# Performance work log

Hardware: AMD Instinct MI355X
Metric: run time of the kernel (lower is better)

The kernel has to match this reference:

```python
import jax, jax.numpy as jnp
import numpy as np

N = 20000      # nodes
E = 320000     # edges (before self loops)
IN = 128       # in_channels
HID = 64       # hid_channels
H = 4          # in_head
OUT = 16       # out_channels (classes)
SLOPE = 0.2    # GATv2 leaky_relu negative_slope default


def setup_inputs() -> dict:
    key = jax.random.key(0)
    ks = jax.random.split(key, 40)
    d = {}
    d["x"] = jax.random.normal(ks[0], (N, IN), jnp.float32)
    src = jax.random.randint(ks[1], (E,), 0, N)
    dst = jax.random.randint(ks[2], (E,), 0, N)
    d["edge_index"] = jnp.stack([src, dst]).astype(jnp.int32)
    # (in_ch, out_ch_per_head, heads) for the 4 GATv2Conv layers
    dims = [(IN, HID, H), (H * HID, HID, H), (H * HID, HID, H), (H * HID, OUT, 1)]
    ki = 3
    for li, (ic, oc, h) in enumerate(dims, 1):
        sc = 1.0 / np.sqrt(ic)
        d[f"w{li}l"] = jax.random.normal(ks[ki], (h * oc, ic), jnp.float32) * sc; ki += 1
        d[f"b{li}l"] = jnp.zeros((h * oc,), jnp.float32)
        d[f"w{li}r"] = jax.random.normal(ks[ki], (h * oc, ic), jnp.float32) * sc; ki += 1
        d[f"b{li}r"] = jnp.zeros((h * oc,), jnp.float32)
        d[f"a{li}"] = jax.random.normal(ks[ki], (h, oc), jnp.float32) * (1.0 / np.sqrt(oc)); ki += 1
        # output bias: [h*oc] if concat else [oc]; layer 4 is concat=False
        d[f"bo{li}"] = jnp.zeros((h * oc if li < 4 else oc,), jnp.float32)
    return d


def gatv2_layer(x, src, dst, wl, bl, wr, br, att, bias, heads, oc, concat):
    n = x.shape[0]
    xl = (x @ wl.T + bl).reshape(n, heads, oc)   # source transform
    xr = (x @ wr.T + br).reshape(n, heads, oc)   # target transform
    # per-edge GATv2 attention logit: a^T LeakyReLU(x_l[src] + x_r[dst])
    e = jax.nn.leaky_relu(xl[src] + xr[dst], SLOPE)          # [E,H,C]
    logits = jnp.einsum('ehc,hc->eh', e, att)                # [E,H]
    # segment softmax over incoming edges of each dst node
    m = jax.ops.segment_max(logits, dst, num_segments=n)     # [N,H]
    ex = jnp.exp(logits - m[dst])
    den = jax.ops.segment_sum(ex, dst, num_segments=n)
    alpha = ex / den[dst]                                    # [E,H]
    out = jax.ops.segment_sum(alpha[..., None] * xl[src], dst, num_segments=n)  # [N,H,C]
    out = out.reshape(n, heads * oc) if concat else out.mean(axis=1)
    return out + bias


def reference(x, edge_index,
              w1l, b1l, w1r, b1r, a1, bo1,
              w2l, b2l, w2r, b2r, a2, bo2,
              w3l, b3l, w3r, b3r, a3, bo3,
              w4l, b4l, w4r, b4r, a4, bo4):
    n = x.shape[0]
    loop = jnp.arange(n, dtype=edge_index.dtype)
    src = jnp.concatenate([edge_index[0], loop])  # PyG GATv2Conv adds self loops
    dst = jnp.concatenate([edge_index[1], loop])
    h = gatv2_layer(x, src, dst, w1l, b1l, w1r, b1r, a1, bo1, H, HID, True)
    h = jax.nn.relu(h)
    h = gatv2_layer(h, src, dst, w2l, b2l, w2r, b2r, a2, bo2, H, HID, True)
    h = jax.nn.relu(h)
    h = gatv2_layer(h, src, dst, w3l, b3l, w3r, b3r, a3, bo3, H, HID, True)
    h = jax.nn.relu(h)
    h = gatv2_layer(h, src, dst, w4l, b4l, w4r, b4r, a4, bo4, 1, OUT, False)
    return h
```

## Files before the change

kernel.cpp:

```cpp
#include <hip/hip_runtime.h>
#include <hip/hip_bf16.h>
#include <math.h>

#define NNODES 20000
#define NEDGES 320000
#define ETOT   (NEDGES + NNODES)
#define SLOPE  0.2f
#define MAXDEG 96

typedef __attribute__((ext_vector_type(8))) short bf16x8;
typedef __attribute__((ext_vector_type(4))) float f32x4;

__device__ inline unsigned short bfbits(float f) {
    __hip_bfloat16 h = __float2bfloat16(f);
    unsigned short u;
    __builtin_memcpy(&u, &h, 2);
    return u;
}
__device__ inline float bf2f(unsigned short u) {
    __hip_bfloat16 h;
    __builtin_memcpy(&h, &u, 2);
    return __bfloat162float(h);
}

__global__ void slab_fill(const int* __restrict__ ei, int* __restrict__ fill,
                          int* __restrict__ slab) {
    int idx = blockIdx.x * blockDim.x + threadIdx.x;
    if (idx >= ETOT) return;
    int src, dst;
    if (idx < NEDGES) { src = ei[idx]; dst = ei[NEDGES + idx]; }
    else              { src = idx - NEDGES; dst = src; }
    int pos = atomicAdd(&fill[dst], 1);
    if (pos < MAXDEG) slab[dst * MAXDEG + pos] = src;
}

__global__ void bin_hist(const int* __restrict__ fill, int* __restrict__ bcnt) {
    __shared__ int h[32];
    const int t = threadIdx.x;
    if (t < 32) h[t] = 0;
    __syncthreads();
    int n = blockIdx.x * 256 + t;
    if (n < NNODES) atomicAdd(&h[min(fill[n], 31)], 1);
    __syncthreads();
    if (t < 32 && h[t] > 0) atomicAdd(&bcnt[t], h[t]);
}

__global__ void bin_scan(const int* __restrict__ bcnt, int* __restrict__ bfill) {
    if (threadIdx.x == 0) {
        int run = 0;
        for (int i = 0; i < 32; i++) { bfill[i] = run; run += bcnt[i]; }
    }
}

__global__ void bin_place(const int* __restrict__ fill, int* __restrict__ bfill,
                          int* __restrict__ order) {
    __shared__ int h[32];
    __shared__ int base[32];
    const int t = threadIdx.x;
    if (t < 32) h[t] = 0;
    __syncthreads();
    int n = blockIdx.x * 256 + t;
    int bin = 0, loc = 0;
    if (n < NNODES) {
        bin = min(fill[n], 31);
        loc = atomicAdd(&h[bin], 1);
    }
    __syncthreads();
    if (t < 32) base[t] = (h[t] > 0) ? atomicAdd(&bfill[t], h[t]) : 0;
    __syncthreads();
    if (n < NNODES) order[base[bin] + loc] = n;
}

__global__ void convert_x(const float* __restrict__ x, unsigned short* __restrict__ Ap) {
    int idx = blockIdx.x * 256 + threadIdx.x;
    if (idx >= NNODES * 128) return;
    int m = idx >> 7, k = idx & 127;
    float f = x[idx];
    unsigned short hi = bfbits(f);
    unsigned short lo = bfbits(f - bf2f(hi));
    unsigned short* row = Ap + (size_t)m * 256;
    row[k] = hi; row[128 + k] = lo;
}

__global__ void convert_w(const float* __restrict__ w0, const float* __restrict__ w1,
                          unsigned short* __restrict__ Wp, int K, int n0, int ntot) {
    int idx = blockIdx.x * 256 + threadIdx.x;
    if (idx >= ntot * K) return;
    int n = idx / K, k = idx - n * K;
    float f = (n < n0) ? w0[n * K + k] : w1[(n - n0) * K + k];
    unsigned short hi = bfbits(f);
    unsigned short lo = bfbits(f - bf2f(hi));
    unsigned short* row = Wp + (size_t)n * 2 * K;
    row[k] = hi; row[K + k] = lo;
}

template <int NOUT, int KK>
__global__ __launch_bounds__(64) void gemm_reg(
    const unsigned short* __restrict__ Ap,
    const unsigned short* __restrict__ Wp,
    const float* __restrict__ bias0, const float* __restrict__ bias1,
    float* __restrict__ O0, float* __restrict__ O1)
{
    constexpr int S  = KK / 32;
    constexpr int NF = (NOUT == 512) ? 4 : 2;

    int m0, n0;
    if constexpr (NOUT == 512) {
        const int xcd  = blockIdx.x & 7;
        const int idx  = blockIdx.x >> 3;
        const int nblk = idx & 7;
        const int mg   = idx >> 3;
        const int mp   = mg * 8 + xcd;
        if (mp >= (NNODES + 63) / 64) return;
        m0 = mp * 64;
        n0 = nblk * 64;
    } else {
        m0 = blockIdx.x * 64;
        n0 = 0;
    }

    const int l   = threadIdx.x;
    const int lr  = l & 15;
    const int lkb = (l >> 4) * 16;

    const char* ab = (const char*)Ap;
    const char* bb = (const char*)Wp;

    unsigned aoff[4], boff[NF];
    #pragma unroll
    for (int f = 0; f < 4; f++) {
        int row = min(m0 + f * 16 + lr, NNODES - 1);
        aoff[f] = (unsigned)row * (unsigned)(4 * KK) + (unsigned)lkb;
    }
    #pragma unroll
    for (int f = 0; f < NF; f++) {
        int row = n0 + f * 16 + lr;
        boff[f] = (unsigned)row * (unsigned)(4 * KK) + (unsigned)lkb;
    }

    f32x4 acc[4][NF];
    #pragma unroll
    for (int i = 0; i < 4; i++)
        #pragma unroll
        for (int j = 0; j < NF; j++)
            acc[i][j] = (f32x4){0.f, 0.f, 0.f, 0.f};

    bf16x8 fa[2][8];
    bf16x8 fb[2][2 * NF];

    auto LD = [&](int buf, int s) {
        const unsigned kb = (unsigned)s * 64;
        #pragma unroll
        for (int f = 0; f < 4; f++) {
            fa[buf][f]     = *(const bf16x8*)(ab + aoff[f] + kb);
            fa[buf][4 + f] = *(const bf16x8*)(ab + aoff[f] + (unsigned)(2 * KK) + kb);
        }
        #pragma unroll
        for (int f = 0; f < NF; f++) {
            fb[buf][f]      = *(const bf16x8*)(bb + boff[f] + kb);
            fb[buf][NF + f] = *(const bf16x8*)(bb + boff[f] + (unsigned)(2 * KK) + kb);
        }
    };

    auto COMP = [&](int buf) {
        #pragma unroll
        for (int mi = 0; mi < 4; mi++)
            #pragma unroll
            for (int ni = 0; ni < NF; ni++) {
                acc[mi][ni] = __builtin_amdgcn_mfma_f32_16x16x32_bf16(
                    fa[buf][mi], fb[buf][ni], acc[mi][ni], 0, 0, 0);
                acc[mi][ni] = __builtin_amdgcn_mfma_f32_16x16x32_bf16(
                    fa[buf][mi], fb[buf][NF + ni], acc[mi][ni], 0, 0, 0);
                acc[mi][ni] = __builtin_amdgcn_mfma_f32_16x16x32_bf16(
                    fa[buf][4 + mi], fb[buf][ni], acc[mi][ni], 0, 0, 0);
            }
    };

    LD(0, 0);
    #pragma unroll
    for (int s = 0; s < S; ++s) {
        if (s + 1 < S) LD((s + 1) & 1, s + 1);
        COMP(s & 1);
    }

    #pragma unroll
    for (int mi = 0; mi < 4; mi++) {
        int r0 = m0 + mi * 16 + (l >> 4) * 4;
        #pragma unroll
        for (int ni = 0; ni < NF; ni++) {
            int c = n0 + ni * 16 + (l & 15);
            if constexpr (NOUT == 512) {
                const bool left = (c < 256);
                float*       O  = left ? O0 : O1;
                const int    cc = left ? c : c - 256;
                const float  bv = left ? bias0[cc] : bias1[cc];
                const int head = cc >> 6, ch = cc & 63;
                #pragma unroll
                for (int r = 0; r < 4; r++) {
                    int m = r0 + r;
                    if (m < NNODES)
                        O[((size_t)head * NNODES + m) * 64 + ch] = acc[mi][ni][r] + bv;
                }
            } else {
                const float bv = (c < 16) ? bias0[c] : bias1[c - 16];
                #pragma unroll
                for (int r = 0; r < 4; r++) {
                    int m = r0 + r;
                    if (m < NNODES) O0[(size_t)m * 32 + c] = acc[mi][ni][r] + bv;
                }
            }
        }
    }
}

__device__ inline float edge_score(float4 v, float4 xrv, float4 attv) {
    float tx = v.x + xrv.x; tx = fmaxf(tx, SLOPE * tx);
    float ty = v.y + xrv.y; ty = fmaxf(ty, SLOPE * ty);
    float tz = v.z + xrv.z; tz = fmaxf(tz, SLOPE * tz);
    float tw = v.w + xrv.w; tw = fmaxf(tw, SLOPE * tw);
    float s = attv.x * tx + attv.y * ty + attv.z * tz + attv.w * tw;
    s += __shfl_xor(s, 1, 64);
    s += __shfl_xor(s, 2, 64);
    s += __shfl_xor(s, 4, 64);
    s += __shfl_xor(s, 8, 64);
    return s;
}

__device__ inline void sm_upd(float s, float4 v, bool act,
                              float& m, float& den, float4& acc) {
    float d = s - m;
    bool  r = act && (d > 8.f);
    float e = __expf(r ? -d : d);
    float sc = r ? e : 1.f;
    float pw = act ? (r ? 1.f : e) : 0.f;
    m = r ? s : m;
    den = den * sc + pw;
    acc.x = acc.x * sc + pw * v.x;
    acc.y = acc.y * sc + pw * v.y;
    acc.z = acc.z * sc + pw * v.z;
    acc.w = acc.w * sc + pw * v.w;
}

__device__ inline void sm_merge(float& m0, float& den0, float4& acc0,
                                float m1, float den1, float4 acc1) {
    float nm = fmaxf(m0, m1);
    float sa = __expf(m0 - nm);
    float sb = __expf(m1 - nm);
    den0 = den0 * sa + den1 * sb;
    acc0.x = acc0.x * sa + acc1.x * sb;
    acc0.y = acc0.y * sa + acc1.y * sb;
    acc0.z = acc0.z * sa + acc1.z * sb;
    acc0.w = acc0.w * sa + acc1.w * sb;
    m0 = nm;
}

__global__ __launch_bounds__(64) void gat_attn_head(
    const float* __restrict__ xl, const float* __restrict__ xr,
    const float* __restrict__ att, const float* __restrict__ bo,
    const int* __restrict__ fill, const int* __restrict__ slab,
    const int* __restrict__ order,
    unsigned short* __restrict__ outp)
{
    const int b    = blockIdx.x;
    const int xcd  = b & 7;
    const int head = xcd >> 1;
    const int grp  = (b >> 3) * 2 + (xcd & 1);
    const int lane = threadIdx.x;
    const int sub  = lane >> 4;
    const int c    = lane & 15;

    const int node = order[grp * 4 + sub];
    const unsigned coff = (unsigned)c << 4;

    const char* xlh = (const char*)xl + (size_t)head * (NNODES * 256);
    const char* xrh = (const char*)xr + (size_t)head * (NNODES * 256);

    const float4 attv = *(const float4*)&att[head * 64 + c * 4];
    const float4 xrv  = *(const float4*)(xrh + ((unsigned)node << 8) + coff);
    const float4 bov  = *(const float4*)&bo[head * 64 + c * 4];

    const int  deg = min(fill[node], MAXDEG);
    const int* sl  = slab + node * MAXDEG;

    int maxd = deg;
    maxd = max(maxd, __shfl_xor(maxd, 16, 64));
    maxd = max(maxd, __shfl_xor(maxd, 32, 64));

    float  m0 = -1e30f, m1 = -1e30f, m2 = -1e30f, m3 = -1e30f;
    float  d0 = 0.f, d1 = 0.f, d2 = 0.f, d3 = 0.f;
    float4 a0 = make_float4(0.f, 0.f, 0.f, 0.f);
    float4 a1 = a0, a2 = a0, a3 = a0;

    auto gather = [&](int src) -> float4 {
        return *(const float4*)(xlh + (((unsigned)src << 8) + coff));
    };

    auto batch = [&](float4 v0, float4 v1, float4 v2, float4 v3, int pb) {
        const bool A0 = pb + 0 < deg, A1 = pb + 1 < deg;
        const bool A2 = pb + 2 < deg, A3 = pb + 3 < deg;
        float s0 = edge_score(v0, xrv, attv);
        float s1 = edge_score(v1, xrv, attv);
        float s2 = edge_score(v2, xrv, attv);
        float s3 = edge_score(v3, xrv, attv);
        bool need = (A0 & (s0 - m0 > 8.f)) | (A1 & (s1 - m1 > 8.f)) |
                    (A2 & (s2 - m2 > 8.f)) | (A3 & (s3 - m3 > 8.f));
        if (!__any(need)) {
            float p0 = A0 ? __expf(s0 - m0) : 0.f;
            float p1 = A1 ? __expf(s1 - m1) : 0.f;
            float p2 = A2 ? __expf(s2 - m2) : 0.f;
            float p3 = A3 ? __expf(s3 - m3) : 0.f;
            d0 += p0; d1 += p1; d2 += p2; d3 += p3;
            a0.x += p0 * v0.x; a0.y += p0 * v0.y; a0.z += p0 * v0.z; a0.w += p0 * v0.w;
            a1.x += p1 * v1.x; a1.y += p1 * v1.y; a1.z += p1 * v1.z; a1.w += p1 * v1.w;
            a2.x += p2 * v2.x; a2.y += p2 * v2.y; a2.z += p2 * v2.z; a2.w += p2 * v2.w;
            a3.x += p3 * v3.x; a3.y += p3 * v3.y; a3.z += p3 * v3.z; a3.w += p3 * v3.w;
        } else {
            sm_upd(s0, v0, A0, m0, d0, a0);
            sm_upd(s1, v1, A1, m1, d1, a1);
            sm_upd(s2, v2, A2, m2, d2, a2);
            sm_upd(s3, v3, A3, m3, d3, a3);
        }
    };

    int4 s4 = *(const int4*)sl;
    float4 v0 = gather((0 < deg) ? s4.x : node);
    float4 v1 = gather((1 < deg) ? s4.y : node);
    float4 v2 = gather((2 < deg) ? s4.z : node);
    float4 v3 = gather((3 < deg) ? s4.w : node);
    int pc = 0;
    for (int p = 4; p < maxd; p += 4) {
        int4 t4 = *(const int4*)&sl[p];
        float4 w0 = gather((p + 0 < deg) ? t4.x : node);
        float4 w1 = gather((p + 1 < deg) ? t4.y : node);
        float4 w2 = gather((p + 2 < deg) ? t4.z : node);
        float4 w3 = gather((p + 3 < deg) ? t4.w : node);
        batch(v0, v1, v2, v3, pc);
        v0 = w0; v1 = w1; v2 = w2; v3 = w3;
        pc = p;
    }
    batch(v0, v1, v2, v3, pc);

    sm_merge(m0, d0, a0, m1, d1, a1);
    sm_merge(m2, d2, a2, m3, d3, a3);
    sm_merge(m0, d0, a0, m2, d2, a2);

    float4 o;
    o.x = fmaxf(a0.x / d0 + bov.x, 0.f);
    o.y = fmaxf(a0.y / d0 + bov.y, 0.f);
    o.z = fmaxf(a0.z / d0 + bov.z, 0.f);
    o.w = fmaxf(a0.w / d0 + bov.w, 0.f);

    unsigned short* row = outp + (size_t)node * 512 + head * 64 + c * 4;
    ushort4 hv, lv;
    hv.x = bfbits(o.x); hv.y = bfbits(o.y); hv.z = bfbits(o.z); hv.w = bfbits(o.w);
    lv.x = bfbits(o.x - bf2f(hv.x));
    lv.y = bfbits(o.y - bf2f(hv.y));
    lv.z = bfbits(o.z - bf2f(hv.z));
    lv.w = bfbits(o.w - bf2f(hv.w));
    *(ushort4*)(row)       = hv;
    *(ushort4*)(row + 256) = lv;
}

__global__ __launch_bounds__(128) void gat_attn_final(
    const float* __restrict__ O32,
    const float* __restrict__ att, const float* __restrict__ bo,
    const int* __restrict__ fill, const int* __restrict__ slab,
    float* __restrict__ out)
{
    const int lane = threadIdx.x & 63;
    const int sub  = lane >> 4;
    const int c    = lane & 15;

    const int node = (blockIdx.x * 2 + (threadIdx.x >> 6)) * 4 + sub;
    if (node >= NNODES) return;

    const unsigned coff = (unsigned)c << 2;
    const char*    ob   = (const char*)O32;

    const float attc = att[c];
    const float xrc  = *(const float*)(ob + (((unsigned)node << 7) + 64 + coff));

    const int  deg = min(fill[node], MAXDEG);
    const int* sl  = slab + node * MAXDEG;

    float m0 = -1e30f, m1 = -1e30f, d0 = 0.f, d1 = 0.f, a0 = 0.f, a1 = 0.f;

    int p = 0;
    for (; p + 2 <= deg; p += 2) {
        int srcA = sl[p];
        int srcB = sl[p + 1];
        float vA = *(const float*)(ob + (((unsigned)srcA << 7) + coff));
        float vB = *(const float*)(ob + (((unsigned)srcB << 7) + coff));
        float tA = vA + xrc; tA = fmaxf(tA, SLOPE * tA);
        float tB = vB + xrc; tB = fmaxf(tB, SLOPE * tB);
        float sA = attc * tA;
        float sB = attc * tB;
        sA += __shfl_xor(sA, 1, 64);  sB += __shfl_xor(sB, 1, 64);
        sA += __shfl_xor(sA, 2, 64);  sB += __shfl_xor(sB, 2, 64);
        sA += __shfl_xor(sA, 4, 64);  sB += __shfl_xor(sB, 4, 64);
        sA += __shfl_xor(sA, 8, 64);  sB += __shfl_xor(sB, 8, 64);
        {
            float dd = sA - m0; bool r = dd > 8.f;
            float e = __expf(r ? -dd : dd);
            float sc = r ? e : 1.f, pw = r ? 1.f : e;
            m0 = r ? sA : m0;
            d0 = d0 * sc + pw;
            a0 = a0 * sc + pw * vA;
        }
        {
            float dd = sB - m1; bool r = dd > 8.f;
            float e = __expf(r ? -dd : dd);
            float sc = r ? e : 1.f, pw = r ? 1.f : e;
            m1 = r ? sB : m1;
            d1 = d1 * sc + pw;
            a1 = a1 * sc + pw * vB;
        }
    }
    if (p < deg) {
        int src = sl[p];
        float v = *(const float*)(ob + (((unsigned)src << 7) + coff));
        float t = v + xrc; t = fmaxf(t, SLOPE * t);
        float s = attc * t;
        s += __shfl_xor(s, 1, 64);
        s += __shfl_xor(s, 2, 64);
        s += __shfl_xor(s, 4, 64);
        s += __shfl_xor(s, 8, 64);
        float dd = s - m0; bool r = dd > 8.f;
        float e = __expf(r ? -dd : dd);
        float sc = r ? e : 1.f, pw = r ? 1.f : e;
        m0 = r ? s : m0;
        d0 = d0 * sc + pw;
        a0 = a0 * sc + pw * v;
    }

    float nm = fmaxf(m0, m1);
    float sa = __expf(m0 - nm);
    float sb = __expf(m1 - nm);
    float den = d0 * sa + d1 * sb;
    out[(size_t)node * 16 + c] = (a0 * sa + a1 * sb) / den + bo[c];
}

extern "C" void kernel_launch(void* const* d_in, const int* in_sizes, int n_in,
                              void* d_out, int out_size, void* d_ws, size_t ws_size,
                              hipStream_t stream)
{
    const float* x   = (const float*)d_in[0];
    const int*   ei  = (const int*)d_in[1];
    const float* w1l = (const float*)d_in[2];  const float* b1l = (const float*)d_in[3];
    const float* w1r = (const float*)d_in[4];  const float* b1r = (const float*)d_in[5];
    const float* a1  = (const float*)d_in[6];  const float* bo1 = (const float*)d_in[7];
    const float* w2l = (const float*)d_in[8];  const float* b2l = (const float*)d_in[9];
    const float* w2r = (const float*)d_in[10]; const float* b2r = (const float*)d_in[11];
    const float* a2  = (const float*)d_in[12]; const float* bo2 = (const float*)d_in[13];
    const float* w3l = (const float*)d_in[14]; const float* b3l = (const float*)d_in[15];
    const float* w3r = (const float*)d_in[16]; const float* b3r = (const float*)d_in[17];
    const float* a3  = (const float*)d_in[18]; const float* bo3 = (const float*)d_in[19];
    const float* w4l = (const float*)d_in[20]; const float* b4l = (const float*)d_in[21];
    const float* w4r = (const float*)d_in[22]; const float* b4r = (const float*)d_in[23];
    const float* a4  = (const float*)d_in[24]; const float* bo4 = (const float*)d_in[25];

    char* ws = (char*)d_ws;
    auto carve = [&](size_t bytes) {
        void* p = ws;
        ws += (bytes + 255) & ~(size_t)255;
        return p;
    };
    unsigned short* Ap = (unsigned short*)carve((size_t)NNODES * 512 * sizeof(unsigned short));
    float* xl = (float*)carve((size_t)NNODES * 256 * sizeof(float));
    float* xr = (float*)carve((size_t)NNODES * 256 * sizeof(float));
    float* O32 = xl;
    unsigned short* Wp1 = (unsigned short*)carve((size_t)512 * 256 * sizeof(unsigned short));
    unsigned short* Wp2 = (unsigned short*)carve((size_t)512 * 512 * sizeof(unsigned short));
    unsigned short* Wp3 = (unsigned short*)carve((size_t)512 * 512 * sizeof(unsigned short));
    unsigned short* Wp4 = (unsigned short*)carve((size_t)32 * 512 * sizeof(unsigned short));
    int* fill  = (int*)carve((size_t)NNODES * sizeof(int));
    int* slab  = (int*)carve((size_t)NNODES * MAXDEG * sizeof(int));
    int* bcnt  = (int*)carve(32 * sizeof(int));
    int* bfill = (int*)carve(32 * sizeof(int));
    int* order = (int*)carve((size_t)NNODES * sizeof(int));

    const int eblocks = (ETOT + 255) / 256;
    const int nblocks = (NNODES + 255) / 256;

    convert_x<<<(NNODES * 128 + 255) / 256, 256, 0, stream>>>(x, Ap);
    convert_w<<<(512 * 128 + 255) / 256, 256, 0, stream>>>(w1l, w1r, Wp1, 128, 256, 512);
    convert_w<<<(512 * 256 + 255) / 256, 256, 0, stream>>>(w2l, w2r, Wp2, 256, 256, 512);
    convert_w<<<(512 * 256 + 255) / 256, 256, 0, stream>>>(w3l, w3r, Wp3, 256, 256, 512);
    convert_w<<<(32 * 256 + 255) / 256, 256, 0, stream>>>(w4l, w4r, Wp4, 256, 16, 32);

    hipMemsetAsync(fill, 0, (size_t)NNODES * sizeof(int), stream);
    hipMemsetAsync(bcnt, 0, 32 * sizeof(int), stream);
    slab_fill<<<eblocks, 256, 0, stream>>>(ei, fill, slab);
    bin_hist<<<nblocks, 256, 0, stream>>>(fill, bcnt);
    bin_scan<<<1, 64, 0, stream>>>(bcnt, bfill);
    bin_place<<<nblocks, 256, 0, stream>>>(fill, bfill, order);

    const int g512 = 2560;
    const int g32  = (NNODES + 63) / 64;
    const int ah   = 20000;

    gemm_reg<512, 128><<<g512, 64, 0, stream>>>(Ap, Wp1, b1l, b1r, xl, xr);
    gat_attn_head<<<ah, 64, 0, stream>>>(xl, xr, a1, bo1, fill, slab, order, Ap);

    gemm_reg<512, 256><<<g512, 64, 0, stream>>>(Ap, Wp2, b2l, b2r, xl, xr);
    gat_attn_head<<<ah, 64, 0, stream>>>(xl, xr, a2, bo2, fill, slab, order, Ap);

    gemm_reg<512, 256><<<g512, 64, 0, stream>>>(Ap, Wp3, b3l, b3r, xl, xr);
    gat_attn_head<<<ah, 64, 0, stream>>>(xl, xr, a3, bo3, fill, slab, order, Ap);

    gemm_reg<32, 256><<<g32, 64, 0, stream>>>(Ap, Wp4, b4l, b4r, O32, O32);
    gat_attn_final<<<(NNODES + 7) / 8, 128, 0, stream>>>(O32, a4, bo4, fill, slab, (float*)d_out);
}
```

Baseline: 307.6 us.

## Stage GEMM tiles through LDS with direct global-to-LDS loads across four waves

Replaces the single-wave register-blocked GEMM with a 256-thread block. Its four waves cooperatively stage 64x32 A and B tiles (hi and lo bf16 parts) into double-buffered shared memory using global_load_lds. Each wave then computes a 32x32 sub-tile from LDS. This is meant to cut redundant global loads and raise per-block parallelism, at the cost of a block barrier every k-step. For the 32-wide final layer, half of the waves compute columns that are then discarded.

```diff
diff --git a/kernel.cpp b/kernel.cpp
--- a/kernel.cpp
+++ b/kernel.cpp
@@ -21,6 +21,12 @@
     __hip_bfloat16 h;
     __builtin_memcpy(&h, &u, 2);
     return __bfloat162float(h);
+}
+
+__device__ inline void gload_lds16(const unsigned short* g, unsigned short* s) {
+    __builtin_amdgcn_global_load_lds(
+        (const __attribute__((address_space(1))) unsigned int*)g,
+        (__attribute__((address_space(3))) unsigned int*)s, 16, 0, 0);
 }
 
 __global__ void slab_fill(const int* __restrict__ ei, int* __restrict__ fill,
@@ -95,14 +101,19 @@
 }
 
 template <int NOUT, int KK>
-__global__ __launch_bounds__(64) void gemm_reg(
+__global__ __launch_bounds__(256) void gemm_lds(
     const unsigned short* __restrict__ Ap,
     const unsigned short* __restrict__ Wp,
     const float* __restrict__ bias0, const float* __restrict__ bias1,
     float* __restrict__ O0, float* __restrict__ O1)
 {
-    constexpr int S  = KK / 32;
-    constexpr int NF = (NOUT == 512) ? 4 : 2;
+    constexpr int S   = KK / 32;
+    constexpr int W2K = 2 * KK;
+
+    __shared__ unsigned short AH[2][4 * 512];
+    __shared__ unsigned short AL[2][4 * 512];
+    __shared__ unsigned short BH[2][4 * 512];
+    __shared__ unsigned short BL[2][4 * 512];
 
     int m0, n0;
     if constexpr (NOUT == 512) {
@@ -119,76 +130,80 @@
         n0 = 0;
     }
 
-    const int l   = threadIdx.x;
-    const int lr  = l & 15;
-    const int lkb = (l >> 4) * 16;
-
-    const char* ab = (const char*)Ap;
-    const char* bb = (const char*)Wp;
-
-    unsigned aoff[4], boff[NF];
+    const int tid = threadIdx.x;
+    const int l   = tid & 63;
+    const int wid = tid >> 6;
+    const int wr  = wid >> 1;
+    const int wc  = wid & 1;
+
+    const int srow = l & 15;
+    const int skb  = l >> 4;
+
+    const int arow = min(m0 + wid * 16 + srow, NNODES - 1);
+    const int brow = min(n0 + wid * 16 + srow, NOUT - 1);
+    const unsigned short* ahg = Ap + (size_t)arow * W2K + skb * 8;
+    const unsigned short* alg = ahg + KK;
+    const unsigned short* bhg = Wp + (size_t)brow * W2K + skb * 8;
+    const unsigned short* blg = bhg + KK;
+
+    f32x4 acc[2][2];
     #pragma unroll
-    for (int f = 0; f < 4; f++) {
-        int row = min(m0 + f * 16 + lr, NNODES - 1);
-        aoff[f] = (unsigned)row * (unsigned)(4 * KK) + (unsigned)lkb;
-    }
-    #pragma unroll
-    for (int f = 0; f < NF; f++) {
-        int row = n0 + f * 16 + lr;
-        boff[f] = (unsigned)row * (unsigned)(4 * KK) + (unsigned)lkb;
-    }
-
-    f32x4 acc[4][NF];
-    #pragma unroll
-    for (int i = 0; i < 4; i++)
+    for (int i = 0; i < 2; i++)
         #pragma unroll
-        for (int j = 0; j < NF; j++)
+        for (int j = 0; j < 2; j++)
             acc[i][j] = (f32x4){0.f, 0.f, 0.f, 0.f};
 
-    bf16x8 fa[2][8];
-    bf16x8 fb[2][2 * NF];
-
-    auto LD = [&](int buf, int s) {
-        const unsigned kb = (unsigned)s * 64;
-        #pragma unroll
-        for (int f = 0; f < 4; f++) {
-            fa[buf][f]     = *(const bf16x8*)(ab + aoff[f] + kb);
-            fa[buf][4 + f] = *(const bf16x8*)(ab + aoff[f] + (unsigned)(2 * KK) + kb);
-        }
-        #pragma unroll
-        for (int f = 0; f < NF; f++) {
-            fb[buf][f]      = *(const bf16x8*)(bb + boff[f] + kb);
-            fb[buf][NF + f] = *(const bf16x8*)(bb + boff[f] + (unsigned)(2 * KK) + kb);
-        }
+    auto STAGE = [&](int buf, int k0) {
+        gload_lds16(ahg + k0, &AH[buf][wid * 512]);
+        gload_lds16(alg + k0, &AL[buf][wid * 512]);
+        gload_lds16(bhg + k0, &BH[buf][wid * 512]);
+        gload_lds16(blg + k0, &BL[buf][wid * 512]);
     };
 
-    auto COMP = [&](int buf) {
-        #pragma unroll
-        for (int mi = 0; mi < 4; mi++)
-            #pragma unroll
-            for (int ni = 0; ni < NF; ni++) {
-                acc[mi][ni] = __builtin_amdgcn_mfma_f32_16x16x32_bf16(
-                    fa[buf][mi], fb[buf][ni], acc[mi][ni], 0, 0, 0);
-                acc[mi][ni] = __builtin_amdgcn_mfma_f32_16x16x32_bf16(
-                    fa[buf][mi], fb[buf][NF + ni], acc[mi][ni], 0, 0, 0);
-                acc[mi][ni] = __builtin_amdgcn_mfma_f32_16x16x32_bf16(
-                    fa[buf][4 + mi], fb[buf][ni], acc[mi][ni], 0, 0, 0);
-            }
-    };
-
-    LD(0, 0);
+    const int ra0 = (wr * 2) * 512 + l * 8;
+    const int ra1 = ra0 + 512;
+    const int rb0 = (wc * 2) * 512 + l * 8;
+    const int rb1 = rb0 + 512;
+
+    STAGE(0, 0);
+    __syncthreads();
+
     #pragma unroll
     for (int s = 0; s < S; ++s) {
-        if (s + 1 < S) LD((s + 1) & 1, s + 1);
-        COMP(s & 1);
+        const int buf = s & 1;
+        if (s + 1 < S) STAGE(buf ^ 1, (s + 1) * 32);
+
+        bf16x8 ah0 = *(const bf16x8*)&AH[buf][ra0];
+        bf16x8 ah1 = *(const bf16x8*)&AH[buf][ra1];
+        bf16x8 al0 = *(const bf16x8*)&AL[buf][ra0];
+        bf16x8 al1 = *(const bf16x8*)&AL[buf][ra1];
+        bf16x8 bh0 = *(const bf16x8*)&BH[buf][rb0];
+        bf16x8 bh1 = *(const bf16x8*)&BH[buf][rb1];
+        bf16x8 bl0 = *(const bf16x8*)&BL[buf][rb0];
+        bf16x8 bl1 = *(const bf16x8*)&BL[buf][rb1];
+
+        acc[0][0] = __builtin_amdgcn_mfma_f32_16x16x32_bf16(ah0, bh0, acc[0][0], 0, 0, 0);
+        acc[0][1] = __builtin_amdgcn_mfma_f32_16x16x32_bf16(ah0, bh1, acc[0][1], 0, 0, 0);
+        acc[1][0] = __builtin_amdgcn_mfma_f32_16x16x32_bf16(ah1, bh0, acc[1][0], 0, 0, 0);
+        acc[1][1] = __builtin_amdgcn_mfma_f32_16x16x32_bf16(ah1, bh1, acc[1][1], 0, 0, 0);
+        acc[0][0] = __builtin_amdgcn_mfma_f32_16x16x32_bf16(ah0, bl0, acc[0][0], 0, 0, 0);
+        acc[0][1] = __builtin_amdgcn_mfma_f32_16x16x32_bf16(ah0, bl1, acc[0][1], 0, 0, 0);
+        acc[1][0] = __builtin_amdgcn_mfma_f32_16x16x32_bf16(ah1, bl0, acc[1][0], 0, 0, 0);
+        acc[1][1] = __builtin_amdgcn_mfma_f32_16x16x32_bf16(ah1, bl1, acc[1][1], 0, 0, 0);
+        acc[0][0] = __builtin_amdgcn_mfma_f32_16x16x32_bf16(al0, bh0, acc[0][0], 0, 0, 0);
+        acc[0][1] = __builtin_amdgcn_mfma_f32_16x16x32_bf16(al0, bh1, acc[0][1], 0, 0, 0);
+        acc[1][0] = __builtin_amdgcn_mfma_f32_16x16x32_bf16(al1, bh0, acc[1][0], 0, 0, 0);
+        acc[1][1] = __builtin_amdgcn_mfma_f32_16x16x32_bf16(al1, bh1, acc[1][1], 0, 0, 0);
+
+        __syncthreads();
     }
 
     #pragma unroll
-    for (int mi = 0; mi < 4; mi++) {
-        int r0 = m0 + mi * 16 + (l >> 4) * 4;
+    for (int mi = 0; mi < 2; mi++) {
+        int r0 = m0 + wr * 32 + mi * 16 + (l >> 4) * 4;
         #pragma unroll
-        for (int ni = 0; ni < NF; ni++) {
-            int c = n0 + ni * 16 + (l & 15);
+        for (int ni = 0; ni < 2; ni++) {
+            int c = n0 + wc * 32 + ni * 16 + (l & 15);
             if constexpr (NOUT == 512) {
                 const bool left = (c < 256);
                 float*       O  = left ? O0 : O1;
@@ -202,6 +217,7 @@
                         O[((size_t)head * NNODES + m) * 64 + ch] = acc[mi][ni][r] + bv;
                 }
             } else {
+                if (c >= 32) continue;
                 const float bv = (c < 16) ? bias0[c] : bias1[c - 16];
                 #pragma unroll
                 for (int r = 0; r < 4; r++) {
@@ -499,15 +515,15 @@
     const int g32  = (NNODES + 63) / 64;
     const int ah   = 20000;
 
-    gemm_reg<512, 128><<<g512, 64, 0, stream>>>(Ap, Wp1, b1l, b1r, xl, xr);
+    gemm_lds<512, 128><<<g512, 256, 0, stream>>>(Ap, Wp1, b1l, b1r, xl, xr);
     gat_attn_head<<<ah, 64, 0, stream>>>(xl, xr, a1, bo1, fill, slab, order, Ap);
 
-    gemm_reg<512, 256><<<g512, 64, 0, stream>>>(Ap, Wp2, b2l, b2r, xl, xr);
+    gemm_lds<512, 256><<<g512, 256, 0, stream>>>(Ap, Wp2, b2l, b2r, xl, xr);
     gat_attn_head<<<ah, 64, 0, stream>>>(xl, xr, a2, bo2, fill, slab, order, Ap);
 
-    gemm_reg<512, 256><<<g512, 64, 0, stream>>>(Ap, Wp3, b3l, b3r, xl, xr);
+    gemm_lds<512, 256><<<g512, 256, 0, stream>>>(Ap, Wp3, b3l, b3r, xl, xr);
     gat_attn_head<<<ah, 64, 0, stream>>>(xl, xr, a3, bo3, fill, slab, order, Ap);
 
-    gemm_reg<32, 256><<<g32, 64, 0, stream>>>(Ap, Wp4, b4l, b4r, O32, O32);
+    gemm_lds<32, 256><<<g32, 256, 0, stream>>>(Ap, Wp4, b4l, b4r, O32, O32);
     gat_attn_final<<<(NNODES + 7) / 8, 128, 0, stream>>>(O32, a4, bo4, fill, slab, (float*)d_out);
 }
```

Result: no change. 310.0 us (+0.8%).
